# Kernel optimization log

Hardware: AMD Instinct MI355X
Metric: run time of the kernel (lower is better)

## Reference

```python
import jax, jax.numpy as jnp
import numpy as np

D_IN, H1, H2, N_CLS, BATCH = 1024, 2048, 2048, 1000, 8192


def setup_inputs() -> dict:
    key = jax.random.key(0)
    ks = jax.random.split(key, 7)
    x = jax.random.normal(ks[0], (BATCH, D_IN), dtype=jnp.float32)
    # torch.nn.Linear default init scale ~ 1/sqrt(fan_in); weights stored [out, in]
    W1 = jax.random.normal(ks[1], (H1, D_IN), dtype=jnp.float32) / np.sqrt(D_IN).astype(np.float32)
    b1 = jax.random.normal(ks[2], (H1,), dtype=jnp.float32) * 0.01
    W2 = jax.random.normal(ks[3], (H2, H1), dtype=jnp.float32) / np.sqrt(H1).astype(np.float32)
    b2 = jax.random.normal(ks[4], (H2,), dtype=jnp.float32) * 0.01
    W3 = jax.random.normal(ks[5], (N_CLS, H2), dtype=jnp.float32) / np.sqrt(H2).astype(np.float32)
    b3 = jax.random.normal(ks[6], (N_CLS,), dtype=jnp.float32) * 0.01
    return {"x": x, "W1": W1, "b1": b1, "W2": W2, "b2": b2, "W3": W3, "b3": b3}


def reference(x, W1, b1, W2, b2, W3, b3):
    # forward_with_coactivations: classifier = [Linear, ReLU, Linear, ReLU, Linear]
    # activation points: the two ReLU layers and the final Linear.
    prev_act = (x > 0).astype(jnp.float32)  # [B, D_IN]

    z1 = x @ W1.T + b1                      # [B, H1]
    a1 = jax.nn.relu(z1)
    act1 = (z1 > 0).astype(jnp.float32)     # (relu(z)>0) == (z>0)
    # sum_s outer(prev_act[s], act1[s]) == prev_act.T @ act1
    coact0 = jnp.einsum('bi,bj->ij', prev_act, act1)  # [D_IN, H1]

    z2 = a1 @ W2.T + b2                     # [B, H2]
    a2 = jax.nn.relu(z2)
    act2 = (z2 > 0).astype(jnp.float32)
    coact1 = jnp.einsum('bi,bj->ij', act1, act2)      # [H1, H2]

    logits = a2 @ W3.T + b3                 # [B, N_CLS]
    act3 = (logits > 0).astype(jnp.float32)
    coact2 = jnp.einsum('bi,bj->ij', act2, act3)      # [H2, N_CLS]

    return logits, coact0, coact1, coact2
```

## Files before the change

### kernel.cpp

```cpp
#include <hip/hip_runtime.h>
#include <hip/hip_bf16.h>


typedef short v8s __attribute__((ext_vector_type(8)));
typedef float v4f __attribute__((ext_vector_type(4)));
typedef int v4i __attribute__((ext_vector_type(4)));

enum { MODE_RELU = 0, MODE_LOGITS = 1 };

__device__ __forceinline__ void async_cp16(const void* gsrc, void* ldst) {
  __builtin_amdgcn_global_load_lds(
      (const __attribute__((address_space(1))) void*)gsrc,
      (__attribute__((address_space(3))) void*)ldst, 16, 0, 0);
}

template <int MODE, int WT>
__global__ __launch_bounds__(256) void gemm_nt(
    const __hip_bfloat16* __restrict__ A, const __hip_bfloat16* __restrict__ B,
    const float* __restrict__ bias, void* __restrict__ Cout,
    char* __restrict__ Tout, int M, int N, int K, int n_store, int ldc) {
  __shared__ char smem[32768];
  __hip_bfloat16* sA = (__hip_bfloat16*)smem;
  __hip_bfloat16* sB = (__hip_bfloat16*)(smem + 16384);
  const int t = threadIdx.x;
  const int m0 = blockIdx.y * 128;
  const int n0 = blockIdx.x * 128;

  const __hip_bfloat16* aG[4];
  const __hip_bfloat16* bG[4];
  char* lA[4];
  char* lB[4];
#pragma unroll
  for (int j = 0; j < 4; j++) {
    const int c = j * 256 + t;
    const int row = c >> 3;
    const int g = (c & 7) ^ (row & 7);
    aG[j] = A + (size_t)(m0 + row) * K + g * 8;
    bG[j] = B + (size_t)(n0 + row) * K + g * 8;
    lA[j] = (char*)sA + c * 16;
    lB[j] = (char*)sB + c * 16;
  }

  const int lane = t & 63;
  const int wave = t >> 6;
  const int wm = (wave & 1) * 64;
  const int wn = (wave >> 1) * 64;
  const int lrow = lane & 15;
  const int quad = lane >> 4;

  const int g0 = quad ^ (lrow & 7);
  const __hip_bfloat16* pa0 = sA + (wm + lrow) * 64 + g0 * 8;
  const __hip_bfloat16* pa1 = sA + (wm + lrow) * 64 + (g0 ^ 4) * 8;
  const __hip_bfloat16* pb0 = sB + (wn + lrow) * 64 + g0 * 8;
  const __hip_bfloat16* pb1 = sB + (wn + lrow) * 64 + (g0 ^ 4) * 8;

  v4f acc[4][4] = {};

  for (int k0 = 0; k0 < K; k0 += 64) {
#pragma unroll
    for (int j = 0; j < 4; j++) {
      async_cp16(aG[j] + k0, lA[j]);
      async_cp16(bG[j] + k0, lB[j]);
    }
    __syncthreads();

    v8s a0[4], b0[4], a1[4], b1[4];
#pragma unroll
    for (int i = 0; i < 4; i++) {
      a0[i] = *(const v8s*)(pa0 + i * 16 * 64);
      b0[i] = *(const v8s*)(pb0 + i * 16 * 64);
    }
#pragma unroll
    for (int mi = 0; mi < 4; mi++)
#pragma unroll
      for (int ni = 0; ni < 4; ni++)
        acc[mi][ni] = __builtin_amdgcn_mfma_f32_16x16x32_bf16(
            a0[mi], b0[ni], acc[mi][ni], 0, 0, 0);
#pragma unroll
    for (int i = 0; i < 4; i++) {
      a1[i] = *(const v8s*)(pa1 + i * 16 * 64);
      b1[i] = *(const v8s*)(pb1 + i * 16 * 64);
    }
#pragma unroll
    for (int mi = 0; mi < 4; mi++)
#pragma unroll
      for (int ni = 0; ni < 4; ni++)
        acc[mi][ni] = __builtin_amdgcn_mfma_f32_16x16x32_bf16(
            a1[mi], b1[ni], acc[mi][ni], 0, 0, 0);
    __syncthreads();
  }

  float bvv[4];
#pragma unroll
  for (int ni = 0; ni < 4; ni++) {
    const int col = n0 + wn + ni * 16 + lrow;
    bvv[ni] = 0.f;
    if (MODE == MODE_RELU) bvv[ni] = bias[col];
    else if (col < n_store) bvv[ni] = bias[col];
  }

#pragma unroll
  for (int ni = 0; ni < 4; ni++) {
    const int col = n0 + wn + ni * 16 + lrow;
#pragma unroll
    for (int mi = 0; mi < 4; mi++) {
      const int rowb = m0 + wm + mi * 16 + quad * 4;
#pragma unroll
      for (int r = 0; r < 4; r++) {
        const int row = rowb + r;
        const float v = acc[mi][ni][r] + bvv[ni];
        if (MODE == MODE_RELU) {
          ((__hip_bfloat16*)Cout)[(size_t)row * ldc + col] =
              __float2bfloat16(v > 0.f ? v : 0.f);
        } else {
          if (col < n_store)
            ((float*)Cout)[(size_t)row * ldc + col] = v;
        }
      }
    }
  }

  if (WT) {
    char* sT = smem;
#pragma unroll
    for (int ni = 0; ni < 4; ni++) {
      const int c = wn + ni * 16 + lrow;
#pragma unroll
      for (int mi = 0; mi < 4; mi++) {
        const int r = wm + mi * 16 + quad * 4;
        char4 bits;
        bits.x = (acc[mi][ni][0] + bvv[ni] > 0.f) ? 1 : 0;
        bits.y = (acc[mi][ni][1] + bvv[ni] > 0.f) ? 1 : 0;
        bits.z = (acc[mi][ni][2] + bvv[ni] > 0.f) ? 1 : 0;
        bits.w = (acc[mi][ni][3] + bvv[ni] > 0.f) ? 1 : 0;
        *(char4*)&sT[c * 144 + r] = bits;
      }
    }
    __syncthreads();
    const int c2 = t >> 1;
    const int hf = (t & 1) * 64;
    char* dst = Tout + (size_t)(n0 + c2) * 8192 + m0 + hf;
    const char* src = sT + c2 * 144 + hf;
#pragma unroll
    for (int j = 0; j < 4; j++)
      *(int4*)(dst + j * 16) = *(const int4*)(src + j * 16);
  }
}

__global__ __launch_bounds__(256) void gemm_nt_i8(
    const char* __restrict__ A, const char* __restrict__ B,
    float* __restrict__ P, int M, int N, int Kc, int n_store, size_t slice) {
  __shared__ char sA[128 * 128];
  __shared__ char sB[128 * 128];
  const int t = threadIdx.x;
  const int m0 = blockIdx.y * 128;
  const int n0 = blockIdx.x * 128;
  const int kbeg = blockIdx.z * Kc;
  const int kend = kbeg + Kc;
  const size_t K = (size_t)Kc * gridDim.z;
  float* __restrict__ Pz = P + (size_t)blockIdx.z * slice;

  const char* aG[4];
  const char* bG[4];
  char* lA[4];
  char* lB[4];
#pragma unroll
  for (int j = 0; j < 4; j++) {
    const int c = j * 256 + t;
    const int row = c >> 3;
    const int g = (c & 7) ^ (row & 7);
    aG[j] = A + (size_t)(m0 + row) * K + g * 16;
    bG[j] = B + (size_t)(n0 + row) * K + g * 16;
    lA[j] = sA + c * 16;
    lB[j] = sB + c * 16;
  }

  const int lane = t & 63;
  const int wave = t >> 6;
  const int wm = (wave & 1) * 64;
  const int wn = (wave >> 1) * 64;
  const int lrow = lane & 15;
  const int quad = lane >> 4;

  const int g0 = quad ^ (lrow & 7);
  const char* pa0 = sA + (wm + lrow) * 128 + g0 * 16;
  const char* pa1 = sA + (wm + lrow) * 128 + (g0 ^ 4) * 16;
  const char* pb0 = sB + (wn + lrow) * 128 + g0 * 16;
  const char* pb1 = sB + (wn + lrow) * 128 + (g0 ^ 4) * 16;

  v4i acc[4][4] = {};

  for (int k0 = kbeg; k0 < kend; k0 += 128) {
#pragma unroll
    for (int j = 0; j < 4; j++) {
      async_cp16(aG[j] + k0, lA[j]);
      async_cp16(bG[j] + k0, lB[j]);
    }
    __syncthreads();

    v4i a0[4], b0[4], a1[4], b1[4];
#pragma unroll
    for (int i = 0; i < 4; i++) {
      a0[i] = *(const v4i*)(pa0 + i * 16 * 128);
      b0[i] = *(const v4i*)(pb0 + i * 16 * 128);
    }
#pragma unroll
    for (int mi = 0; mi < 4; mi++)
#pragma unroll
      for (int ni = 0; ni < 4; ni++)
        acc[mi][ni] = __builtin_amdgcn_mfma_i32_16x16x64_i8(
            a0[mi], b0[ni], acc[mi][ni], 0, 0, 0);
#pragma unroll
    for (int i = 0; i < 4; i++) {
      a1[i] = *(const v4i*)(pa1 + i * 16 * 128);
      b1[i] = *(const v4i*)(pb1 + i * 16 * 128);
    }
#pragma unroll
    for (int mi = 0; mi < 4; mi++)
#pragma unroll
      for (int ni = 0; ni < 4; ni++)
        acc[mi][ni] = __builtin_amdgcn_mfma_i32_16x16x64_i8(
            a1[mi], b1[ni], acc[mi][ni], 0, 0, 0);
    __syncthreads();
  }

#pragma unroll
  for (int ni = 0; ni < 4; ni++) {
    const int col = n0 + wn + ni * 16 + lrow;
    if (col >= n_store) continue;
#pragma unroll
    for (int mi = 0; mi < 4; mi++) {
      const int rowb = m0 + wm + mi * 16 + quad * 4;
#pragma unroll
      for (int r = 0; r < 4; r++) {
        Pz[(size_t)(rowb + r) * n_store + col] = (float)acc[mi][ni][r];
      }
    }
  }
}

template <int Z>
__global__ __launch_bounds__(256) void reduce_part(
    const float* __restrict__ P, float* __restrict__ out, int n4, size_t slice) {
  const int i = blockIdx.x * 256 + threadIdx.x;
  if (i >= n4) return;
  float4 s = ((const float4*)P)[i];
#pragma unroll
  for (int z = 1; z < Z; z++) {
    const float4 v = ((const float4*)(P + (size_t)z * slice))[i];
    s.x += v.x; s.y += v.y; s.z += v.z; s.w += v.w;
  }
  ((float4*)out)[i] = s;
}

__global__ __launch_bounds__(256) void transpose_bin8f(
    const float* __restrict__ in, char* __restrict__ out,
    int R, int ldin, int Cphys) {
  __shared__ char tile[64][65];
  const int c0 = blockIdx.x * 64;
  const int r0 = blockIdx.y * 64;
  const int tx = threadIdx.x & 63;
  const int ty = threadIdx.x >> 6;
#pragma unroll
  for (int i = 0; i < 64; i += 4) {
    const int c = c0 + tx;
    const int r = r0 + ty + i;
    float v = 0.f;
    if (c < Cphys) v = in[(size_t)r * ldin + c];
    tile[ty + i][tx] = (v > 0.f) ? 1 : 0;
  }
  __syncthreads();
  const int u = threadIdx.x & 15;
  const int cg = threadIdx.x >> 4;
#pragma unroll
  for (int i = 0; i < 64; i += 16) {
    const int col = cg + i;
    char4 v;
    v.x = tile[4 * u + 0][col];
    v.y = tile[4 * u + 1][col];
    v.z = tile[4 * u + 2][col];
    v.w = tile[4 * u + 3][col];
    *(char4*)&out[(size_t)(c0 + col) * R + r0 + 4 * u] = v;
  }
}

struct Cvt4 {
  const float* src[4];
  __hip_bfloat16* dst[4];
  int n4[4];
};
__global__ __launch_bounds__(256) void f32_to_bf16_multi(Cvt4 c) {
  int i = blockIdx.x * 256 + threadIdx.x;
#pragma unroll
  for (int s = 0; s < 4; s++) {
    if (i < c.n4[s]) {
      const float4 v = ((const float4*)c.src[s])[i];
      union { __hip_bfloat16 h[4]; ushort4 u; } cv;
      cv.h[0] = __float2bfloat16(v.x);
      cv.h[1] = __float2bfloat16(v.y);
      cv.h[2] = __float2bfloat16(v.z);
      cv.h[3] = __float2bfloat16(v.w);
      ((ushort4*)c.dst[s])[i] = cv.u;
      return;
    }
    i -= c.n4[s];
  }
}

extern "C" void kernel_launch(void* const* d_in, const int* in_sizes, int n_in,
                              void* d_out, int out_size, void* d_ws, size_t ws_size,
                              hipStream_t stream) {
  const float* x  = (const float*)d_in[0];
  const float* W1 = (const float*)d_in[1];
  const float* b1 = (const float*)d_in[2];
  const float* W2 = (const float*)d_in[3];
  const float* b2 = (const float*)d_in[4];
  const float* W3 = (const float*)d_in[5];
  const float* b3 = (const float*)d_in[6];

  float* logits = (float*)d_out;
  float* coact0 = logits + (size_t)8192 * 1000;
  float* coact1 = coact0 + (size_t)1024 * 2048;
  float* coact2 = coact1 + (size_t)2048 * 2048;

  char* ws = (char*)d_ws;
  size_t off = 0;
  auto alloc = [&](size_t bytes) {
    char* p = ws + off;
    off += (bytes + 255) & ~(size_t)255;
    return p;
  };
  __hip_bfloat16* X   = (__hip_bfloat16*)alloc((size_t)8192 * 1024 * 2);
  __hip_bfloat16* W1b = (__hip_bfloat16*)alloc((size_t)2048 * 1024 * 2);
  __hip_bfloat16* W2b = (__hip_bfloat16*)alloc((size_t)2048 * 2048 * 2);
  __hip_bfloat16* W3b = (__hip_bfloat16*)alloc((size_t)1024 * 2048 * 2);
  __hip_bfloat16* A1  = (__hip_bfloat16*)alloc((size_t)8192 * 2048 * 2);
  __hip_bfloat16* A2  = (__hip_bfloat16*)alloc((size_t)8192 * 2048 * 2);
  char* T0 = (char*)alloc((size_t)1024 * 8192);
  char* T1 = (char*)alloc((size_t)2048 * 8192);
  char* T2 = (char*)X;
  char* T3 = (char*)W2b;
  float* P = (float*)A1;

  const dim3 blk(256);

  {
    Cvt4 c;
    c.src[0] = x;  c.dst[0] = X;   c.n4[0] = 8192 * 1024 / 4;
    c.src[1] = W1; c.dst[1] = W1b; c.n4[1] = 2048 * 1024 / 4;
    c.src[2] = W2; c.dst[2] = W2b; c.n4[2] = 2048 * 2048 / 4;
    c.src[3] = W3; c.dst[3] = W3b; c.n4[3] = 1000 * 2048 / 4;
    const int total = c.n4[0] + c.n4[1] + c.n4[2] + c.n4[3];
    f32_to_bf16_multi<<<(total + 255) / 256, blk, 0, stream>>>(c);
  }

  transpose_bin8f<<<dim3(16, 128), blk, 0, stream>>>(x, T0, 8192, 1024, 1024);

  gemm_nt<MODE_RELU, 1><<<dim3(16, 64), blk, 0, stream>>>(
      X, W1b, b1, A1, T1, 8192, 2048, 1024, 2048, 2048);

  gemm_nt<MODE_RELU, 1><<<dim3(16, 64), blk, 0, stream>>>(
      A1, W2b, b2, A2, T2, 8192, 2048, 2048, 2048, 2048);

  gemm_nt<MODE_LOGITS, 1><<<dim3(8, 64), blk, 0, stream>>>(
      A2, W3b, b3, logits, T3, 8192, 1024, 2048, 1000, 1000);

  gemm_nt_i8<<<dim3(16, 8, 4), blk, 0, stream>>>(T0, T1, P,
                                                 1024, 2048, 2048, 2048,
                                                 (size_t)1024 * 2048);
  reduce_part<4><<<1024 * 2048 / 4 / 256, blk, 0, stream>>>(
      P, coact0, 1024 * 2048 / 4, (size_t)1024 * 2048);

  gemm_nt_i8<<<dim3(16, 16, 2), blk, 0, stream>>>(T1, T2, P,
                                                  2048, 2048, 4096, 2048,
                                                  (size_t)2048 * 2048);
  reduce_part<2><<<2048 * 2048 / 4 / 256, blk, 0, stream>>>(
      P, coact1, 2048 * 2048 / 4, (size_t)2048 * 2048);

  gemm_nt_i8<<<dim3(8, 16, 4), blk, 0, stream>>>(T2, T3, P,
                                                 2048, 1024, 2048, 1000,
                                                 (size_t)2048 * 1000);
  reduce_part<4><<<2048 * 1000 / 4 / 256, blk, 0, stream>>>(
      P, coact2, 2048 * 1000 / 4, (size_t)2048 * 1000);
}
```

Before: 444.5 us.

## Add 256x256-tile 8-wave pipelined bf16 GEMM for the two hidden ReLU layers

```diff
diff --git a/kernel.cpp b/kernel.cpp
--- a/kernel.cpp
+++ b/kernel.cpp
@@ -12,6 +12,255 @@
   __builtin_amdgcn_global_load_lds(
       (const __attribute__((address_space(1))) void*)gsrc,
       (__attribute__((address_space(3))) void*)ldst, 16, 0, 0);
+}
+
+#define FENCE asm volatile("" ::: "memory")
+#define BAR()                         \
+  do {                                \
+    FENCE;                            \
+    __builtin_amdgcn_s_barrier();     \
+    FENCE;                            \
+  } while (0)
+#define WAITL()                                          \
+  do {                                                   \
+    asm volatile("s_waitcnt lgkmcnt(0)" ::: "memory");   \
+    __builtin_amdgcn_sched_barrier(0);                   \
+  } while (0)
+#define WAITV(n)                                           \
+  do {                                                     \
+    asm volatile("s_waitcnt vmcnt(" #n ")" ::: "memory");  \
+    __builtin_amdgcn_sched_barrier(0);                     \
+  } while (0)
+#define PRIO1 __builtin_amdgcn_s_setprio(1)
+#define PRIO0 __builtin_amdgcn_s_setprio(0)
+
+__global__ __launch_bounds__(512, 2) void gemm256_relu_wt(
+    const __hip_bfloat16* __restrict__ A, const __hip_bfloat16* __restrict__ B,
+    const float* __restrict__ bias, __hip_bfloat16* __restrict__ Cout,
+    char* __restrict__ Tout, int K, int ldc) {
+  __shared__ char smem[131072];
+  const int t = threadIdx.x;
+  const int m0 = blockIdx.y * 256;
+  const int n0 = blockIdx.x * 256;
+
+  const int c0 = t, c1 = 512 + t;
+  const int r0s = c0 >> 3, r1s = c1 >> 3;
+  const int goff0 = r0s * K + ((c0 & 7) ^ (r0s & 7)) * 8;
+  const int goff1 = r1s * K + ((c1 & 7) ^ (r1s & 7)) * 8;
+  const int loff0 = c0 * 16, loff1 = c1 * 16;
+
+  const __hip_bfloat16* const Abase = A + (size_t)m0 * K;
+  const __hip_bfloat16* const Bbase = B + (size_t)n0 * K;
+  const size_t hk = (size_t)128 * K;
+
+  char* const pA0l = smem;
+  char* const pA0h = smem + 16384;
+  char* const pB0l = smem + 32768;
+  char* const pB0h = smem + 49152;
+  char* const pA1l = smem + 65536;
+  char* const pA1h = smem + 81920;
+  char* const pB1l = smem + 98304;
+  char* const pB1h = smem + 114688;
+
+  const int lane = t & 63;
+  const int wave = t >> 6;
+  const int wm = wave >> 2;
+  const int wn = wave & 3;
+  const int lrow = lane & 15;
+  const int quad = lane >> 4;
+  const int sl0 = ((quad ^ (lrow & 7)) * 16);
+  const int sl1 = (((quad + 4) ^ (lrow & 7)) * 16);
+  const int ardA = (wm * 128 + lrow) * 128;
+  const int ardB = (wn * 64 + lrow) * 128;
+
+  v4f acc[8][4] = {};
+  v8s alo[4][2], ahi[4][2], blo[2][2], bhi[2][2];
+
+#define STAGE(dst, src)                                          \
+  do {                                                           \
+    async_cp16((const void*)((src) + goff0), (void*)((dst) + loff0)); \
+    async_cp16((const void*)((src) + goff1), (void*)((dst) + loff1)); \
+  } while (0)
+
+#define LDA_H(dst, hh, bb)                                                   \
+  _Pragma("unroll") for (int mi = 0; mi < 4; mi++) {                         \
+    dst[mi][0] =                                                             \
+        *(const v8s*)(smem + (bb) + ardA + (hh)*8192 + mi * 2048 + sl0);     \
+    dst[mi][1] =                                                             \
+        *(const v8s*)(smem + (bb) + ardA + (hh)*8192 + mi * 2048 + sl1);     \
+  }
+
+#define LDB_P(dst, pp, bb)                                                    \
+  _Pragma("unroll") for (int ni = 0; ni < 2; ni++) {                          \
+    dst[ni][0] = *(const v8s*)(smem + (bb) + 32768 + ardB +                   \
+                               ((pp)*2 + ni) * 2048 + sl0);                   \
+    dst[ni][1] = *(const v8s*)(smem + (bb) + 32768 + ardB +                   \
+                               ((pp)*2 + ni) * 2048 + sl1);                   \
+  }
+
+#define MMA_Q(af, bf, MB, NB)                                               \
+  _Pragma("unroll") for (int mi = 0; mi < 4; mi++)                          \
+      _Pragma("unroll") for (int ni = 0; ni < 2; ni++)                      \
+          _Pragma("unroll") for (int ks = 0; ks < 2; ks++)                  \
+              acc[(MB) + mi][(NB) + ni] =                                   \
+      __builtin_amdgcn_mfma_f32_16x16x32_bf16(                              \
+          af[mi][ks], bf[ni][ks], acc[(MB) + mi][(NB) + ni], 0, 0, 0);
+
+  STAGE(pA0l, Abase);
+  STAGE(pA0h, Abase + hk);
+  STAGE(pB0l, Bbase);
+  STAGE(pB0h, Bbase + hk);
+  STAGE(pA1l, Abase + 64);
+  STAGE(pA1h, Abase + hk + 64);
+  WAITV(4);
+  BAR();
+
+  const int NI = K >> 7;
+#pragma unroll 1
+  for (int i = 0; i < NI - 1; ++i) {
+    const int k1 = (2 * i + 1) << 6;
+    const int k2 = (2 * i + 2) << 6;
+    const int k3 = (2 * i + 3) << 6;
+    LDA_H(alo, 0, 0);
+    LDB_P(blo, 0, 0);
+    STAGE(pB1l, Bbase + k1);
+    BAR();
+    WAITL();
+    PRIO1; MMA_Q(alo, blo, 0, 0); PRIO0;
+    BAR();
+    LDA_H(ahi, 1, 0);
+    STAGE(pB1h, Bbase + hk + k1);
+    BAR();
+    WAITL();
+    PRIO1; MMA_Q(ahi, blo, 4, 0); PRIO0;
+    BAR();
+    LDB_P(bhi, 1, 0);
+    STAGE(pA0l, Abase + k2);
+    BAR();
+    WAITL();
+    PRIO1; MMA_Q(alo, bhi, 0, 2); PRIO0;
+    BAR();
+    STAGE(pA0h, Abase + hk + k2);
+    BAR();
+    PRIO1; MMA_Q(ahi, bhi, 4, 2); PRIO0;
+    WAITV(4);
+    BAR();
+    LDA_H(alo, 0, 65536);
+    LDB_P(blo, 0, 65536);
+    STAGE(pB0l, Bbase + k2);
+    BAR();
+    WAITL();
+    PRIO1; MMA_Q(alo, blo, 0, 0); PRIO0;
+    BAR();
+    LDA_H(ahi, 1, 65536);
+    STAGE(pB0h, Bbase + hk + k2);
+    BAR();
+    WAITL();
+    PRIO1; MMA_Q(ahi, blo, 4, 0); PRIO0;
+    BAR();
+    LDB_P(bhi, 1, 65536);
+    STAGE(pA1l, Abase + k3);
+    BAR();
+    WAITL();
+    PRIO1; MMA_Q(alo, bhi, 0, 2); PRIO0;
+    BAR();
+    STAGE(pA1h, Abase + hk + k3);
+    BAR();
+    PRIO1; MMA_Q(ahi, bhi, 4, 2); PRIO0;
+    WAITV(4);
+    BAR();
+  }
+  {
+    const int k1 = (2 * (NI - 1) + 1) << 6;
+    LDA_H(alo, 0, 0);
+    LDB_P(blo, 0, 0);
+    STAGE(pB1l, Bbase + k1);
+    BAR();
+    WAITL();
+    PRIO1; MMA_Q(alo, blo, 0, 0); PRIO0;
+    BAR();
+    LDA_H(ahi, 1, 0);
+    STAGE(pB1h, Bbase + hk + k1);
+    BAR();
+    WAITL();
+    PRIO1; MMA_Q(ahi, blo, 4, 0); PRIO0;
+    BAR();
+    LDB_P(bhi, 1, 0);
+    BAR();
+    WAITL();
+    PRIO1; MMA_Q(alo, bhi, 0, 2); PRIO0;
+    BAR();
+    BAR();
+    PRIO1; MMA_Q(ahi, bhi, 4, 2); PRIO0;
+    WAITV(0);
+    BAR();
+    LDA_H(alo, 0, 65536);
+    LDB_P(blo, 0, 65536);
+    BAR();
+    WAITL();
+    PRIO1; MMA_Q(alo, blo, 0, 0); PRIO0;
+    BAR();
+    LDA_H(ahi, 1, 65536);
+    BAR();
+    WAITL();
+    PRIO1; MMA_Q(ahi, blo, 4, 0); PRIO0;
+    BAR();
+    LDB_P(bhi, 1, 65536);
+    BAR();
+    WAITL();
+    PRIO1; MMA_Q(alo, bhi, 0, 2); PRIO0;
+    BAR();
+    BAR();
+    PRIO1; MMA_Q(ahi, bhi, 4, 2); PRIO0;
+    BAR();
+  }
+#undef STAGE
+#undef LDA_H
+#undef LDB_P
+#undef MMA_Q
+
+  float bv[4];
+#pragma unroll
+  for (int ni = 0; ni < 4; ni++) bv[ni] = bias[n0 + wn * 64 + ni * 16 + lrow];
+
+#pragma unroll
+  for (int mi = 0; mi < 8; mi++) {
+    const int rowb = m0 + wm * 128 + mi * 16 + quad * 4;
+#pragma unroll
+    for (int ni = 0; ni < 4; ni++) {
+      const int col = n0 + wn * 64 + ni * 16 + lrow;
+#pragma unroll
+      for (int r = 0; r < 4; r++) {
+        const float v = acc[mi][ni][r] + bv[ni];
+        Cout[(size_t)(rowb + r) * ldc + col] =
+            __float2bfloat16(v > 0.f ? v : 0.f);
+      }
+    }
+  }
+
+  char* const sT = smem;
+#pragma unroll
+  for (int ni = 0; ni < 4; ni++) {
+    const int c = wn * 64 + ni * 16 + lrow;
+#pragma unroll
+    for (int mi = 0; mi < 8; mi++) {
+      const int rw = wm * 128 + mi * 16 + quad * 4;
+      char4 bits;
+      bits.x = (acc[mi][ni][0] + bv[ni] > 0.f) ? 1 : 0;
+      bits.y = (acc[mi][ni][1] + bv[ni] > 0.f) ? 1 : 0;
+      bits.z = (acc[mi][ni][2] + bv[ni] > 0.f) ? 1 : 0;
+      bits.w = (acc[mi][ni][3] + bv[ni] > 0.f) ? 1 : 0;
+      *(char4*)&sT[c * 272 + rw] = bits;
+    }
+  }
+  __syncthreads();
+  const int rw2 = t >> 1;
+  const int hf = (t & 1) * 128;
+  char* dst = Tout + (size_t)(n0 + rw2) * 8192 + m0 + hf;
+  const char* src = sT + rw2 * 272 + hf;
+#pragma unroll
+  for (int j = 0; j < 8; j++)
+    *(int4*)(dst + j * 16) = *(const int4*)(src + j * 16);
 }
 
 template <int MODE, int WT>
@@ -356,11 +605,11 @@
 
   transpose_bin8f<<<dim3(16, 128), blk, 0, stream>>>(x, T0, 8192, 1024, 1024);
 
-  gemm_nt<MODE_RELU, 1><<<dim3(16, 64), blk, 0, stream>>>(
-      X, W1b, b1, A1, T1, 8192, 2048, 1024, 2048, 2048);
-
-  gemm_nt<MODE_RELU, 1><<<dim3(16, 64), blk, 0, stream>>>(
-      A1, W2b, b2, A2, T2, 8192, 2048, 2048, 2048, 2048);
+  gemm256_relu_wt<<<dim3(8, 32), dim3(512), 0, stream>>>(
+      X, W1b, b1, A1, T1, 1024, 2048);
+
+  gemm256_relu_wt<<<dim3(8, 32), dim3(512), 0, stream>>>(
+      A1, W2b, b2, A2, T2, 2048, 2048);
 
   gemm_nt<MODE_LOGITS, 1><<<dim3(8, 64), blk, 0, stream>>>(
       A2, W3b, b3, logits, T3, 8192, 1024, 2048, 1000, 1000);
```

Measured after the change: 429.4 us. -3.4%, faster.
